# Performance work log

Measured on AMD Instinct MI355X. Metric: run time of the kernel, lower is better.

## Reference

```python
import jax, jax.numpy as jnp
import numpy as np

GROUPS = 6  # attn_group in Stack

def setup_inputs() -> dict:
    key = jax.random.key(0)
    k0, k1, k2, k3, k4 = jax.random.split(key, 5)
    B, S, IN, OUT, K = 2, 2048, 512, 768, 31
    fan = (2.0 / IN) ** 0.5  # kaiming_normal fan_out-ish scale
    x = jax.random.normal(k0, (B, S, IN), jnp.float32)
    W_q = jax.random.normal(k1, (OUT, IN), jnp.float32) * fan
    W_k = jax.random.normal(k2, (OUT, IN), jnp.float32) * fan
    W_v = jax.random.normal(k3, (OUT, IN), jnp.float32) * fan
    rel = jax.random.normal(k4, (OUT, K), jnp.float32)
    return {"x": x, "W_q": W_q, "W_k": W_k, "W_v": W_v, "rel": rel}

def reference(x, W_q, W_k, W_v, rel):
    B, S, _ = x.shape
    OUT, K = rel.shape
    pad = (K - 1) // 2
    d = OUT // GROUPS
    # projections
    q = x @ W_q.T                                   # [B,S,OUT]
    xp = jnp.pad(x, ((0, 0), (pad, pad), (0, 0)))    # pad seq dim
    k = xp @ W_k.T                                  # [B,S+K-1,OUT]
    v = xp @ W_v.T
    # unfold: window of size K per query position (stride 1)
    idx = jnp.arange(S)[:, None] + jnp.arange(K)[None, :]   # [S,K]
    k_win = k[:, idx, :] + rel.T                    # [B,S,K,OUT], rel bias (out,K)->(K,out)
    v_win = v[:, idx, :]                            # [B,S,K,OUT]
    k_win = k_win.reshape(B, S, K, GROUPS, d)
    v_win = v_win.reshape(B, S, K, GROUPS, d)
    qg = q.reshape(B, S, GROUPS, d)
    energy = jnp.einsum('bsgd,bskgd->bsgk', qg, k_win)       # QK dot over head dim
    attn = jax.nn.softmax(energy, axis=-1)                   # softmax over window
    out = jnp.einsum('bsgk,bskgd->bsgd', attn, v_win).reshape(B, S, OUT)
    return out, attn  # attn matches torch attention.squeeze(3): [B,S,groups,K]
```

## Files before the change

kernel.cpp:

```cpp
#include <hip/hip_runtime.h>
#include <hip/hip_bf16.h>

#define S_LEN 2048
#define B_SZ 2
#define IN_DIM 512
#define OUT_DIM 768
#define KWIN 31
#define PAD 15
#define NGROUP 6
#define DHEAD 128
#define M_TOT 4096
#define N_TOT 2304
#define QK_W 1536

typedef __attribute__((ext_vector_type(8))) __bf16 bf16x8;
typedef __attribute__((ext_vector_type(8))) unsigned short u16x8;
typedef __attribute__((ext_vector_type(4))) float f32x4;

static __device__ __forceinline__ unsigned short f2bf(float f) {
  unsigned int u = __float_as_uint(f);
  unsigned int r = (u + 0x7fffu + ((u >> 16) & 1u)) >> 16;
  return (unsigned short)r;
}
static __device__ __forceinline__ float bf2f(unsigned short h) {
  return __uint_as_float(((unsigned int)h) << 16);
}

__global__ __launch_bounds__(256) void prep_kernel(
    const float* __restrict__ x,
    const float* __restrict__ Wq, const float* __restrict__ Wk, const float* __restrict__ Wv,
    const float* __restrict__ rel,
    unsigned short* __restrict__ xhi, unsigned short* __restrict__ xlo,
    unsigned short* __restrict__ whi, unsigned short* __restrict__ wlo,
    unsigned short* __restrict__ relThi, unsigned short* __restrict__ relTlo,
    unsigned short* __restrict__ zpage) {
  const int bid = blockIdx.x;
  const int tid = threadIdx.x;
  if (bid < 2048) {
    int i = bid * 256 + tid;
    float4 v = ((const float4*)x)[i];
    unsigned short h0 = f2bf(v.x), h1 = f2bf(v.y), h2 = f2bf(v.z), h3 = f2bf(v.w);
    ((ushort4*)xhi)[i] = make_ushort4(h0, h1, h2, h3);
    ((ushort4*)xlo)[i] = make_ushort4(f2bf(v.x - bf2f(h0)), f2bf(v.y - bf2f(h1)),
                                      f2bf(v.z - bf2f(h2)), f2bf(v.w - bf2f(h3)));
  } else if (bid < 3200) {
    int i = (bid - 2048) * 256 + tid;
    int e = i * 4;
    const int per = OUT_DIM * IN_DIM;
    const float* src = (e < per) ? Wq : (e < 2 * per) ? Wk : Wv;
    int rem = (e < per) ? e : (e < 2 * per) ? e - per : e - 2 * per;
    float4 v = *(const float4*)(src + rem);
    unsigned short h0 = f2bf(v.x), h1 = f2bf(v.y), h2 = f2bf(v.z), h3 = f2bf(v.w);
    ((ushort4*)whi)[i] = make_ushort4(h0, h1, h2, h3);
    ((ushort4*)wlo)[i] = make_ushort4(f2bf(v.x - bf2f(h0)), f2bf(v.y - bf2f(h1)),
                                      f2bf(v.z - bf2f(h2)), f2bf(v.w - bf2f(h3)));
  } else if (bid < 3293) {
    int idx = (bid - 3200) * 256 + tid;
    int kk = idx / OUT_DIM;
    int o = idx - kk * OUT_DIM;
    float v = rel[o * KWIN + kk];
    unsigned short h = f2bf(v);
    relThi[idx] = h;
    relTlo[idx] = f2bf(v - bf2f(h));
  } else {
    if (tid < 128) zpage[tid] = 0;
  }
}

#define SLOTB 49152

static __device__ __forceinline__ int swz32(int O) {
  return O ^ (((O >> 7) & 3) << 4);
}

#define MFMA16(AF, BF) \
  _Pragma("unroll") for (int mi = 0; mi < 4; ++mi) \
  _Pragma("unroll") for (int ni = 0; ni < 4; ++ni) \
    acc[mi][ni] = __builtin_amdgcn_mfma_f32_16x16x32_bf16( \
        AF[mi], BF[ni], acc[mi][ni], 0, 0, 0);

#define READ_AHI() _Pragma("unroll") for (int mi = 0; mi < 4; ++mi) ahi[mi] = *(const bf16x8*)(slot + aoff[mi]);
#define READ_ALO() _Pragma("unroll") for (int mi = 0; mi < 4; ++mi) alo[mi] = *(const bf16x8*)(slot + 16384 + aoff[mi]);
#define READ_WHI() _Pragma("unroll") for (int ni = 0; ni < 4; ++ni) whi[ni] = *(const bf16x8*)(slot + 32768 + boff[ni]);
#define READ_WLO() _Pragma("unroll") for (int ni = 0; ni < 4; ++ni) wlo[ni] = *(const bf16x8*)(slot + 40960 + boff[ni]);

#define END_BARRIER() \
  __builtin_amdgcn_s_barrier(); \
  asm volatile("" ::: "memory");

__global__ __launch_bounds__(512, 2) void gemm_kernel(
    const unsigned short* __restrict__ Ahi, const unsigned short* __restrict__ Alo,
    const unsigned short* __restrict__ Whi, const unsigned short* __restrict__ Wlo,
    unsigned short* __restrict__ qkhi, unsigned short* __restrict__ qklo,
    unsigned short* __restrict__ vTw) {
  __shared__ unsigned short lds_u16[73728];
  char* ldsb = (char*)lds_u16;
  const int tid = threadIdx.x;
  const int wid = tid >> 6, lane = tid & 63;
  const int elr = lane & 15, elq = lane >> 4;
  const int wm = wid >> 1, wn = wid & 1;

  int aoff[4], boff[4];
#pragma unroll
  for (int mi = 0; mi < 4; ++mi)
    aoff[mi] = swz32((wm * 64 + mi * 16 + elr) * 64 + elq * 16);
#pragma unroll
  for (int ni = 0; ni < 4; ++ni)
    boff[ni] = swz32((wn * 64 + ni * 16 + elr) * 64 + elq * 16);

  const int strow = tid >> 2;
  const int stcol = (((tid & 3) ^ ((tid >> 3) & 3)) << 3);

  auto stage8k = [&](char* slot, int RO, int j, const unsigned short* src,
                     int grow0, int kloc) {
    const unsigned short* g = src + (size_t)(grow0 + j * 128 + strow) * IN_DIM + kloc + stcol;
    __builtin_amdgcn_global_load_lds((const __attribute__((address_space(1))) void*)g,
        (__attribute__((address_space(3))) void*)(slot + RO + j * 8192 + wid * 1024), 16, 0, 0);
  };

  f32x4 acc[4][4] = {};
  bf16x8 ahi[4], whi[4], alo[4], wlo[4];

  const int bid = blockIdx.x;

  if (bid < 192) {
    const int bm = bid & 15, ct = bid >> 4;
    const int row0 = bm << 8, col0 = ct << 7;

    auto stageChunk = [&](int cc) {
      char* s = ldsb + (cc % 3) * SLOTB;
      const int pk = cc << 5;
      stage8k(s, 0, 0, Ahi, row0, pk);      stage8k(s, 0, 1, Ahi, row0, pk);
      stage8k(s, 16384, 0, Alo, row0, pk);  stage8k(s, 16384, 1, Alo, row0, pk);
      stage8k(s, 32768, 0, Whi, col0, pk);  stage8k(s, 40960, 0, Wlo, col0, pk);
    };

    stageChunk(0);
    stageChunk(1);
    asm volatile("s_waitcnt vmcnt(6)" ::: "memory");
    END_BARRIER()

    for (int c = 0; c < 16; ++c) {
      char* slot = ldsb + (c % 3) * SLOTB;
      const bool pref = (c + 2) < 16;
      if (pref) stageChunk(c + 2);
      READ_AHI()
      READ_WHI()
      READ_ALO()
      READ_WLO()
      __builtin_amdgcn_s_setprio(1);
      MFMA16(ahi, whi)
      MFMA16(alo, whi)
      MFMA16(ahi, wlo)
      __builtin_amdgcn_s_setprio(0);
      if (pref) { asm volatile("s_waitcnt vmcnt(6)" ::: "memory"); }
      else      { asm volatile("s_waitcnt vmcnt(0)" ::: "memory"); }
      END_BARRIER()
    }

    const int elg = elq * 4;
#pragma unroll
    for (int mi = 0; mi < 4; ++mi)
#pragma unroll
      for (int ni = 0; ni < 4; ++ni) {
        int ncol = col0 + wn * 64 + ni * 16 + elr;
        size_t rbase = (size_t)(row0 + wm * 64 + mi * 16 + elg);
#pragma unroll
        for (int j = 0; j < 4; ++j) {
          float v = acc[mi][ni][j];
          unsigned short h = f2bf(v);
          size_t idx = (rbase + j) * QK_W + ncol;
          qkhi[idx] = h;
          qklo[idx] = f2bf(v - bf2f(h));
        }
      }
  } else {
    const int bid2 = bid - 192;
    const int bm = bid2 & 15, grp = bid2 >> 4;
    const int row0 = bm << 8;
    auto vcol = [&](int ci) { return 1536 + ((grp * 2 + (ci >> 4)) << 7); };

    auto stageChunkV = [&](int cc) {
      char* s = ldsb + (cc % 3) * SLOTB;
      const int pk = (cc & 15) << 5;
      stage8k(s, 0, 0, Ahi, row0, pk);  stage8k(s, 0, 1, Ahi, row0, pk);
      stage8k(s, 32768, 0, Whi, vcol(cc), pk);
    };

    stageChunkV(0);
    stageChunkV(1);
    asm volatile("s_waitcnt vmcnt(3)" ::: "memory");
    END_BARRIER()

    for (int ci = 0; ci < 32; ++ci) {
      char* slot = ldsb + (ci % 3) * SLOTB;
      const bool pref = (ci + 2) < 32;
      if (pref) stageChunkV(ci + 2);
      READ_AHI()
      READ_WHI()
      __builtin_amdgcn_s_setprio(1);
      MFMA16(ahi, whi)
      __builtin_amdgcn_s_setprio(0);
      if (pref) { asm volatile("s_waitcnt vmcnt(3)" ::: "memory"); }
      else      { asm volatile("s_waitcnt vmcnt(0)" ::: "memory"); }
      END_BARRIER()

      if ((ci & 15) == 15) {
        const int col0 = vcol(ci);
        const int elg = elq * 4;
#pragma unroll
        for (int mi = 0; mi < 4; ++mi)
#pragma unroll
          for (int ni = 0; ni < 4; ++ni) {
            int d = col0 - 1536 + wn * 64 + ni * 16 + elr;
            int srw = row0 + wm * 64 + mi * 16 + elg;
            ushort4 pk4;
            pk4.x = f2bf(acc[mi][ni][0]); pk4.y = f2bf(acc[mi][ni][1]);
            pk4.z = f2bf(acc[mi][ni][2]); pk4.w = f2bf(acc[mi][ni][3]);
            *(ushort4*)(vTw + (size_t)d * M_TOT + srw) = pk4;
            acc[mi][ni] = (f32x4){0.f, 0.f, 0.f, 0.f};
          }
      }
    }
  }
}

__global__ __launch_bounds__(256, 2) void attn_kernel(
    const unsigned short* __restrict__ qkhi, const unsigned short* __restrict__ qklo,
    const unsigned short* __restrict__ vT,
    const unsigned short* __restrict__ relThi, const unsigned short* __restrict__ relTlo,
    const unsigned short* __restrict__ zpage,
    float* __restrict__ out, float* __restrict__ attn_out) {
  __shared__ __attribute__((aligned(16))) unsigned short smem[40960];
  char* smb = (char*)smem;
  float* Elds = (float*)(smb + 69632);

  const int tid = threadIdx.x;
  const int wid = tid >> 6, lane = tid & 63;
  const int bid = (blockIdx.x & 7) * 96 + (blockIdx.x >> 3);
  const int tile = bid & 63;
  const int g = (bid >> 6) % NGROUP;
  const int b = bid / (64 * NGROUP);
  const int s0 = tile * 32;
  const size_t rowbase = (size_t)b * S_LEN;
  const int elr = lane & 15, elq = lane >> 4;

  {
    const int wrow = wid * 4 + (lane >> 4);
    const int kcb = lane & 15;
#pragma unroll
    for (int arr = 0; arr < 2; ++arr) {
      const unsigned short* src = arr ? qklo : qkhi;
      const unsigned short* rsrc = arr ? relTlo : relThi;
      const int ldsbase = arr ? 24576 : 0;
#pragma unroll
      for (int i = 0; i < 6; ++i) {
        int w = i * 16 + wrow;
        int scb = (kcb ^ (w & 7)) * 8;
        const unsigned short* gp;
        if (w < 62) {
          int r = s0 - 15 + w;
          gp = (r >= 0 && r < S_LEN)
             ? src + (size_t)(rowbase + r) * QK_W + OUT_DIM + g * DHEAD + scb
             : zpage + scb;
        } else if (w < 93) {
          gp = rsrc + (w - 62) * OUT_DIM + g * DHEAD + scb;
        } else {
          gp = zpage + scb;
        }
        __builtin_amdgcn_global_load_lds((const __attribute__((address_space(1))) void*)gp,
            (__attribute__((address_space(3))) void*)(smb + ldsbase + (i * 16 + wid * 4) * 256 + (lane & 15) * 16 + (lane >> 4) * 256),
            16, 0, 0);
      }
    }
  }
  {
    const unsigned short* vsrc = vT + (size_t)g * DHEAD * M_TOT + (size_t)b * S_LEN;
    const int drow = wid * 8 + (lane >> 3);
    const int vcb = lane & 7;
#pragma unroll
    for (int i = 0; i < 4; ++i) {
      int d = i * 32 + drow;
      int sl = s0 - 16 + (vcb ^ (d & 7)) * 8;
      const unsigned short* gp = (sl >= 0 && sl < S_LEN)
        ? vsrc + (size_t)d * M_TOT + sl
        : zpage + (vcb ^ (d & 7)) * 8;
      __builtin_amdgcn_global_load_lds((const __attribute__((address_space(1))) void*)gp,
          (__attribute__((address_space(3))) void*)(smb + 49152 + (i * 32 + wid * 8) * 128 + (lane >> 3) * 128 + (lane & 7) * 16),
          16, 0, 0);
    }
  }
  {
    int O = tid * 16;
    O ^= (O >> 3) & 0x70;
    u16x8 z = {};
    *(u16x8*)(smb + 65536 + O) = z;
  }

  const int rf = wid & 1;
  const int cb3 = 3 * (wid >> 1);
  bf16x8 qh[4], ql[4];
  {
    size_t qrow = rowbase + s0 + rf * 16 + elr;
    const unsigned short* qb  = qkhi + qrow * QK_W + g * DHEAD + elq * 8;
    const unsigned short* qb2 = qklo + qrow * QK_W + g * DHEAD + elq * 8;
#pragma unroll
    for (int ks = 0; ks < 4; ++ks) {
      qh[ks] = *(const bf16x8*)(qb + ks * 32);
      ql[ks] = *(const bf16x8*)(qb2 + ks * 32);
    }
  }
  __syncthreads();

#pragma unroll
  for (int cf = 0; cf < 3; ++cf) {
    int c = cb3 + cf;
    f32x4 ea = {};
#pragma unroll
    for (int ks = 0; ks < 4; ++ks) {
      int O = (c * 16 + elr) * 256 + ks * 64 + elq * 16;
      int Os = O ^ ((O >> 4) & 0x70);
      bf16x8 kh = *(const bf16x8*)(smb + Os);
      bf16x8 kl = *(const bf16x8*)(smb + 24576 + Os);
      __builtin_amdgcn_s_setprio(1);
      ea = __builtin_amdgcn_mfma_f32_16x16x32_bf16(qh[ks], kh, ea, 0, 0, 0);
      ea = __builtin_amdgcn_mfma_f32_16x16x32_bf16(ql[ks], kh, ea, 0, 0, 0);
      ea = __builtin_amdgcn_mfma_f32_16x16x32_bf16(qh[ks], kl, ea, 0, 0, 0);
      __builtin_amdgcn_s_setprio(0);
    }
#pragma unroll
    for (int j = 0; j < 4; ++j)
      Elds[(rf * 16 + elq * 4 + j) * 96 + c * 16 + elr] = ea[j];
  }
  __syncthreads();

  {
    const int kkl = lane & 31;
    const int half = lane >> 5;
    const int kkc = (kkl < 31) ? kkl : 30;
#pragma unroll
    for (int p = 0; p < 4; ++p) {
      int si = p * 8 + wid * 2 + half;
      float e = Elds[si * 96 + si + kkc] + Elds[si * 96 + 62 + kkc];
      if (kkl == 31) e = -INFINITY;
      float m = e;
#pragma unroll
      for (int off = 16; off > 0; off >>= 1) m = fmaxf(m, __shfl_xor(m, off, 32));
      float pr = __expf(e - m);
      float sum = pr;
#pragma unroll
      for (int off = 16; off > 0; off >>= 1) sum += __shfl_xor(sum, off, 32);
      float a = pr / sum;
      if (kkl < 31) {
        attn_out[((rowbase + s0 + si) * NGROUP + g) * KWIN + kkl] = a;
        int O = si * 128 + (si + kkl + 1) * 2;
        O ^= (O >> 3) & 0x70;
        *(unsigned short*)(smb + 65536 + O) = f2bf(a);
      }
    }
  }
  __syncthreads();

  {
    const int pcb = 4 * (wid >> 1);
    f32x4 pa[4] = {};
#pragma unroll
    for (int ks = 0; ks < 2; ++ks) {
      int AO = (rf * 16 + elr) * 128 + ks * 64 + elq * 16;
      AO ^= (AO >> 3) & 0x70;
      bf16x8 afr = *(const bf16x8*)(smb + 65536 + AO);
      __builtin_amdgcn_s_setprio(1);
#pragma unroll
      for (int cf = 0; cf < 4; ++cf) {
        int VO = ((pcb + cf) * 16 + elr) * 128 + ks * 64 + elq * 16;
        VO ^= (VO >> 3) & 0x70;
        bf16x8 vfr = *(const bf16x8*)(smb + 49152 + VO);
        pa[cf] = __builtin_amdgcn_mfma_f32_16x16x32_bf16(afr, vfr, pa[cf], 0, 0, 0);
      }
      __builtin_amdgcn_s_setprio(0);
    }
#pragma unroll
    for (int cf = 0; cf < 4; ++cf)
#pragma unroll
      for (int j = 0; j < 4; ++j)
        out[(rowbase + s0 + rf * 16 + elq * 4 + j) * OUT_DIM + g * DHEAD + pcb * 16 + cf * 16 + elr]
            = pa[cf][j];
  }
}

extern "C" void kernel_launch(void* const* d_in, const int* in_sizes, int n_in,
                              void* d_out, int out_size, void* d_ws, size_t ws_size,
                              hipStream_t stream) {
  const float* x   = (const float*)d_in[0];
  const float* Wq  = (const float*)d_in[1];
  const float* Wk  = (const float*)d_in[2];
  const float* Wv  = (const float*)d_in[3];
  const float* rel = (const float*)d_in[4];

  char* ws = (char*)d_ws;
  unsigned short* Ahi    = (unsigned short*)(ws);
  unsigned short* Alo    = (unsigned short*)(ws + 4194304);
  unsigned short* Whi    = (unsigned short*)(ws + 8388608);
  unsigned short* Wlo    = (unsigned short*)(ws + 10747904);
  unsigned short* relThi = (unsigned short*)(ws + 13107200);
  unsigned short* relTlo = (unsigned short*)(ws + 13154816);
  unsigned short* qkhi   = (unsigned short*)(ws + 13202432);
  unsigned short* qklo   = (unsigned short*)(ws + 25785344);
  unsigned short* vTw    = (unsigned short*)(ws + 38368256);
  unsigned short* zpage  = (unsigned short*)(ws + 44659712);

  float* outp = (float*)d_out;
  float* attn = outp + (size_t)B_SZ * S_LEN * OUT_DIM;

  prep_kernel<<<3294, 256, 0, stream>>>(x, Wq, Wk, Wv, rel, Ahi, Alo, Whi, Wlo,
                                        relThi, relTlo, zpage);
  gemm_kernel<<<240, 512, 0, stream>>>(Ahi, Alo, Whi, Wlo, qkhi, qklo, vTw);
  attn_kernel<<<768, 256, 0, stream>>>(qkhi, qklo, vTw, relThi, relTlo, zpage, outp, attn);
}
```

Baseline: 56.45 us.

## Shrink attention LDS footprint to raise occupancy, reorder GEMM prefetch after reads

The attention kernel's LDS drops from 80KB to 45KB. The low-half K is now read directly from global memory into registers instead of being staged in LDS. The V tile is loaded after softmax into the region freed by the energy buffer, and launch bounds are raised to 3 blocks per CU. In the projection GEMM loops, the next-chunk prefetch is issued after the LDS fragment reads instead of before. The trade-offs are uncoalesced global loads for K-lo, V loads that no longer overlap the QK phase, and added register pressure from the higher occupancy target.

```diff
diff --git a/kernel.cpp b/kernel.cpp
--- a/kernel.cpp
+++ b/kernel.cpp
@@ -142,12 +142,12 @@
 
     for (int c = 0; c < 16; ++c) {
       char* slot = ldsb + (c % 3) * SLOTB;
-      const bool pref = (c + 2) < 16;
-      if (pref) stageChunk(c + 2);
       READ_AHI()
       READ_WHI()
       READ_ALO()
       READ_WLO()
+      const bool pref = (c + 2) < 16;
+      if (pref) stageChunk(c + 2);
       __builtin_amdgcn_s_setprio(1);
       MFMA16(ahi, whi)
       MFMA16(alo, whi)
@@ -194,10 +194,10 @@
 
     for (int ci = 0; ci < 32; ++ci) {
       char* slot = ldsb + (ci % 3) * SLOTB;
+      READ_AHI()
+      READ_WHI()
       const bool pref = (ci + 2) < 32;
       if (pref) stageChunkV(ci + 2);
-      READ_AHI()
-      READ_WHI()
       __builtin_amdgcn_s_setprio(1);
       MFMA16(ahi, whi)
       __builtin_amdgcn_s_setprio(0);
@@ -225,15 +225,17 @@
   }
 }
 
-__global__ __launch_bounds__(256, 2) void attn_kernel(
+__global__ __launch_bounds__(256, 3) void attn_kernel(
     const unsigned short* __restrict__ qkhi, const unsigned short* __restrict__ qklo,
     const unsigned short* __restrict__ vT,
     const unsigned short* __restrict__ relThi, const unsigned short* __restrict__ relTlo,
     const unsigned short* __restrict__ zpage,
     float* __restrict__ out, float* __restrict__ attn_out) {
-  __shared__ __attribute__((aligned(16))) unsigned short smem[40960];
+  __shared__ __attribute__((aligned(16))) unsigned short smem[22528];
   char* smb = (char*)smem;
-  float* Elds = (float*)(smb + 69632);
+  float* Elds = (float*)(smb + 24576);
+  const int VT_BASE = 24576;
+  const int AB_BASE = 40960;
 
   const int tid = threadIdx.x;
   const int wid = tid >> 6, lane = tid & 63;
@@ -249,31 +251,110 @@
     const int wrow = wid * 4 + (lane >> 4);
     const int kcb = lane & 15;
 #pragma unroll
-    for (int arr = 0; arr < 2; ++arr) {
-      const unsigned short* src = arr ? qklo : qkhi;
-      const unsigned short* rsrc = arr ? relTlo : relThi;
-      const int ldsbase = arr ? 24576 : 0;
-#pragma unroll
-      for (int i = 0; i < 6; ++i) {
-        int w = i * 16 + wrow;
-        int scb = (kcb ^ (w & 7)) * 8;
-        const unsigned short* gp;
-        if (w < 62) {
-          int r = s0 - 15 + w;
-          gp = (r >= 0 && r < S_LEN)
-             ? src + (size_t)(rowbase + r) * QK_W + OUT_DIM + g * DHEAD + scb
-             : zpage + scb;
-        } else if (w < 93) {
-          gp = rsrc + (w - 62) * OUT_DIM + g * DHEAD + scb;
-        } else {
-          gp = zpage + scb;
-        }
-        __builtin_amdgcn_global_load_lds((const __attribute__((address_space(1))) void*)gp,
-            (__attribute__((address_space(3))) void*)(smb + ldsbase + (i * 16 + wid * 4) * 256 + (lane & 15) * 16 + (lane >> 4) * 256),
-            16, 0, 0);
+    for (int i = 0; i < 6; ++i) {
+      int w = i * 16 + wrow;
+      int scb = (kcb ^ (w & 7)) * 8;
+      const unsigned short* gp;
+      if (w < 62) {
+        int r = s0 - 15 + w;
+        gp = (r >= 0 && r < S_LEN)
+           ? qkhi + (size_t)(rowbase + r) * QK_W + OUT_DIM + g * DHEAD + scb
+           : zpage + scb;
+      } else if (w < 93) {
+        gp = relThi + (w - 62) * OUT_DIM + g * DHEAD + scb;
+      } else {
+        gp = zpage + scb;
       }
-    }
-  }
+      __builtin_amdgcn_global_load_lds((const __attribute__((address_space(1))) void*)gp,
+          (__attribute__((address_space(3))) void*)(smb + (i * 16 + wid * 4) * 256 + (lane & 15) * 16 + (lane >> 4) * 256),
+          16, 0, 0);
+    }
+  }
+  {
+    int O = tid * 16;
+    O ^= (O >> 3) & 0x70;
+    u16x8 z = {};
+    *(u16x8*)(smb + AB_BASE + O) = z;
+  }
+
+  const int rf = wid & 1;
+  const int cb3 = 3 * (wid >> 1);
+  bf16x8 qh[4], ql[4];
+  {
+    size_t qrow = rowbase + s0 + rf * 16 + elr;
+    const unsigned short* qb  = qkhi + qrow * QK_W + g * DHEAD + elq * 8;
+    const unsigned short* qb2 = qklo + qrow * QK_W + g * DHEAD + elq * 8;
+#pragma unroll
+    for (int ks = 0; ks < 4; ++ks) {
+      qh[ks] = *(const bf16x8*)(qb + ks * 32);
+      ql[ks] = *(const bf16x8*)(qb2 + ks * 32);
+    }
+  }
+  __syncthreads();
+
+#pragma unroll
+  for (int cf = 0; cf < 3; ++cf) {
+    int c = cb3 + cf;
+    const unsigned short* klbase;
+    {
+      int w = c * 16 + elr;
+      int r = s0 - 15 + w;
+      if (w < 62)      klbase = (r >= 0 && r < S_LEN)
+                                ? qklo + (size_t)(rowbase + r) * QK_W + OUT_DIM + g * DHEAD
+                                : zpage;
+      else if (w < 93) klbase = relTlo + (w - 62) * OUT_DIM + g * DHEAD;
+      else             klbase = zpage;
+    }
+    bf16x8 kl[4];
+#pragma unroll
+    for (int ks = 0; ks < 4; ++ks)
+      kl[ks] = *(const bf16x8*)(klbase + ks * 32 + elq * 8);
+
+    f32x4 ea = {};
+#pragma unroll
+    for (int ks = 0; ks < 4; ++ks) {
+      int O = (c * 16 + elr) * 256 + ks * 64 + elq * 16;
+      int Os = O ^ ((O >> 4) & 0x70);
+      bf16x8 kh = *(const bf16x8*)(smb + Os);
+      __builtin_amdgcn_s_setprio(1);
+      ea = __builtin_amdgcn_mfma_f32_16x16x32_bf16(qh[ks], kh, ea, 0, 0, 0);
+      ea = __builtin_amdgcn_mfma_f32_16x16x32_bf16(ql[ks], kh, ea, 0, 0, 0);
+      ea = __builtin_amdgcn_mfma_f32_16x16x32_bf16(qh[ks], kl[ks], ea, 0, 0, 0);
+      __builtin_amdgcn_s_setprio(0);
+    }
+#pragma unroll
+    for (int j = 0; j < 4; ++j)
+      Elds[(rf * 16 + elq * 4 + j) * 96 + c * 16 + elr] = ea[j];
+  }
+  __syncthreads();
+
+  {
+    const int kkl = lane & 31;
+    const int half = lane >> 5;
+    const int kkc = (kkl < 31) ? kkl : 30;
+#pragma unroll
+    for (int p = 0; p < 4; ++p) {
+      int si = p * 8 + wid * 2 + half;
+      float e = Elds[si * 96 + si + kkc] + Elds[si * 96 + 62 + kkc];
+      if (kkl == 31) e = -INFINITY;
+      float m = e;
+#pragma unroll
+      for (int off = 16; off > 0; off >>= 1) m = fmaxf(m, __shfl_xor(m, off, 32));
+      float pr = __expf(e - m);
+      float sum = pr;
+#pragma unroll
+      for (int off = 16; off > 0; off >>= 1) sum += __shfl_xor(sum, off, 32);
+      float a = pr / sum;
+      if (kkl < 31) {
+        attn_out[((rowbase + s0 + si) * NGROUP + g) * KWIN + kkl] = a;
+        int O = si * 128 + (si + kkl + 1) * 2;
+        O ^= (O >> 3) & 0x70;
+        *(unsigned short*)(smb + AB_BASE + O) = f2bf(a);
+      }
+    }
+  }
+  __syncthreads();
+
   {
     const unsigned short* vsrc = vT + (size_t)g * DHEAD * M_TOT + (size_t)b * S_LEN;
     const int drow = wid * 8 + (lane >> 3);
@@ -286,77 +367,8 @@
         ? vsrc + (size_t)d * M_TOT + sl
         : zpage + (vcb ^ (d & 7)) * 8;
       __builtin_amdgcn_global_load_lds((const __attribute__((address_space(1))) void*)gp,
-          (__attribute__((address_space(3))) void*)(smb + 49152 + (i * 32 + wid * 8) * 128 + (lane >> 3) * 128 + (lane & 7) * 16),
+          (__attribute__((address_space(3))) void*)(smb + VT_BASE + (i * 32 + wid * 8) * 128 + (lane >> 3) * 128 + (lane & 7) * 16),
           16, 0, 0);
-    }
-  }
-  {
-    int O = tid * 16;
-    O ^= (O >> 3) & 0x70;
-    u16x8 z = {};
-    *(u16x8*)(smb + 65536 + O) = z;
-  }
-
-  const int rf = wid & 1;
-  const int cb3 = 3 * (wid >> 1);
-  bf16x8 qh[4], ql[4];
-  {
-    size_t qrow = rowbase + s0 + rf * 16 + elr;
-    const unsigned short* qb  = qkhi + qrow * QK_W + g * DHEAD + elq * 8;
-    const unsigned short* qb2 = qklo + qrow * QK_W + g * DHEAD + elq * 8;
-#pragma unroll
-    for (int ks = 0; ks < 4; ++ks) {
-      qh[ks] = *(const bf16x8*)(qb + ks * 32);
-      ql[ks] = *(const bf16x8*)(qb2 + ks * 32);
-    }
-  }
-  __syncthreads();
-
-#pragma unroll
-  for (int cf = 0; cf < 3; ++cf) {
-    int c = cb3 + cf;
-    f32x4 ea = {};
-#pragma unroll
-    for (int ks = 0; ks < 4; ++ks) {
-      int O = (c * 16 + elr) * 256 + ks * 64 + elq * 16;
-      int Os = O ^ ((O >> 4) & 0x70);
-      bf16x8 kh = *(const bf16x8*)(smb + Os);
-      bf16x8 kl = *(const bf16x8*)(smb + 24576 + Os);
-      __builtin_amdgcn_s_setprio(1);
-      ea = __builtin_amdgcn_mfma_f32_16x16x32_bf16(qh[ks], kh, ea, 0, 0, 0);
-      ea = __builtin_amdgcn_mfma_f32_16x16x32_bf16(ql[ks], kh, ea, 0, 0, 0);
-      ea = __builtin_amdgcn_mfma_f32_16x16x32_bf16(qh[ks], kl, ea, 0, 0, 0);
-      __builtin_amdgcn_s_setprio(0);
-    }
-#pragma unroll
-    for (int j = 0; j < 4; ++j)
-      Elds[(rf * 16 + elq * 4 + j) * 96 + c * 16 + elr] = ea[j];
-  }
-  __syncthreads();
-
-  {
-    const int kkl = lane & 31;
-    const int half = lane >> 5;
-    const int kkc = (kkl < 31) ? kkl : 30;
-#pragma unroll
-    for (int p = 0; p < 4; ++p) {
-      int si = p * 8 + wid * 2 + half;
-      float e = Elds[si * 96 + si + kkc] + Elds[si * 96 + 62 + kkc];
-      if (kkl == 31) e = -INFINITY;
-      float m = e;
-#pragma unroll
-      for (int off = 16; off > 0; off >>= 1) m = fmaxf(m, __shfl_xor(m, off, 32));
-      float pr = __expf(e - m);
-      float sum = pr;
-#pragma unroll
-      for (int off = 16; off > 0; off >>= 1) sum += __shfl_xor(sum, off, 32);
-      float a = pr / sum;
-      if (kkl < 31) {
-        attn_out[((rowbase + s0 + si) * NGROUP + g) * KWIN + kkl] = a;
-        int O = si * 128 + (si + kkl + 1) * 2;
-        O ^= (O >> 3) & 0x70;
-        *(unsigned short*)(smb + 65536 + O) = f2bf(a);
-      }
     }
   }
   __syncthreads();
@@ -368,13 +380,13 @@
     for (int ks = 0; ks < 2; ++ks) {
       int AO = (rf * 16 + elr) * 128 + ks * 64 + elq * 16;
       AO ^= (AO >> 3) & 0x70;
-      bf16x8 afr = *(const bf16x8*)(smb + 65536 + AO);
+      bf16x8 afr = *(const bf16x8*)(smb + AB_BASE + AO);
       __builtin_amdgcn_s_setprio(1);
 #pragma unroll
       for (int cf = 0; cf < 4; ++cf) {
         int VO = ((pcb + cf) * 16 + elr) * 128 + ks * 64 + elq * 16;
         VO ^= (VO >> 3) & 0x70;
-        bf16x8 vfr = *(const bf16x8*)(smb + 49152 + VO);
+        bf16x8 vfr = *(const bf16x8*)(smb + VT_BASE + VO);
         pa[cf] = __builtin_amdgcn_mfma_f32_16x16x32_bf16(afr, vfr, pa[cf], 0, 0, 0);
       }
       __builtin_amdgcn_s_setprio(0);
```

New measurement: 53.45 us. 5.3% less time.
